# Kernel optimization log

Hardware: AMD Instinct MI355X
Metric: run time of the kernel (lower is better)

## Reference

```python
import jax, jax.numpy as jnp
import numpy as np


def setup_inputs() -> dict:
    key = jax.random.key(0)
    ks = jax.random.split(key, 5)
    T, C_IN, C_OUT, H = 1024, 4, 2, 32
    x = jax.random.normal(ks[0], (T, C_IN), dtype=jnp.float32)
    # timestamps (relative positions); arange normalized to [0,1)
    t = jnp.arange(T, dtype=jnp.float32) / T
    # KernelNet params: Linear(3,H) -> Sine -> Linear(H,1)
    w1 = jax.random.normal(ks[1], (H, 3), dtype=jnp.float32) * (1.0 / np.sqrt(3.0))
    b1 = jax.random.normal(ks[2], (H,), dtype=jnp.float32) * 0.1
    w2 = jax.random.normal(ks[3], (1, H), dtype=jnp.float32) * (1.0 / np.sqrt(H))
    b2 = jax.random.normal(ks[4], (1,), dtype=jnp.float32) * 0.1
    return {"x": x, "t": t, "w1": w1, "b1": b1, "w2": w2, "b2": b2,
            "out_channels": C_OUT}


def reference(x, t, w1, b1, w2, b2, out_channels):
    # x: [T, C_in], t: [T]
    T, C_in = x.shape
    # dt[i, j] = t[j] - t[i]  (rep_t - rep_t.t() in the original)
    dt = t[None, :] - t[:, None]                                  # [T, T]
    # Kernel MLP input is [dt, in_channel_idx, out_channel_idx]; the first
    # Linear layer is affine, so split contributions: dt*w1[:,0] varies over
    # (i, j) while the channel-index part varies only over (o, c).
    h_dt = dt[:, :, None] * w1[:, 0]                              # [T, T, H]
    c_idx = jnp.arange(C_in, dtype=x.dtype)                       # [C_in]
    o_idx = jnp.arange(out_channels, dtype=x.dtype)               # [C_out]
    off = (o_idx[:, None, None] * w1[:, 2]
           + c_idx[None, :, None] * w1[:, 1]
           + b1)                                                  # [O, C, H]
    h = jnp.sin(h_dt[None, None] + off[:, :, None, None, :])      # [O, C, T, T, H]
    kernel = jnp.einsum('ocijh,h->ocij', h, w2[0]) + b2[0]        # [O, C, T, T]
    # causal mask: keep entries with j <= i (lower triangular), tiled per (o, c)
    mask = jnp.tril(jnp.ones((T, T), dtype=x.dtype))
    kernel = kernel * mask
    # y[i, o] = sum_{c, j<=i} kernel[o, c, i, j] * x[j, c]
    return jnp.einsum('ocij,jc->io', kernel, x)                   # [T, O]
```

## Files before the change

kernel.cpp:

```cpp
#include <hip/hip_runtime.h>
#include <math.h>

__global__ void ck_build_kernel_table(const float* __restrict__ t,
                                      const float* __restrict__ w1,
                                      const float* __restrict__ b1,
                                      const float* __restrict__ w2,
                                      const float* __restrict__ b2,
                                      float* __restrict__ Kt,
                                      int T, int Cin, int Cout, int H) {
    int idx = blockIdx.x * blockDim.x + threadIdx.x;
    int total = T * Cout * Cin;
    if (idx >= total) return;
    int oc  = Cout * Cin;
    int d   = idx / oc;
    int rem = idx - d * oc;
    int o   = rem / Cin;
    int c   = rem - o * Cin;

    float dt = t[0] - t[d];
    float fo = (float)o;
    float fc = (float)c;

    float acc = 0.0f;
    for (int h = 0; h < H; ++h) {
        float a = dt * w1[h * 3 + 0] + fc * w1[h * 3 + 1] + fo * w1[h * 3 + 2] + b1[h];
        acc += w2[h] * sinf(a);
    }
    Kt[idx] = acc + b2[0];
}

__global__ __launch_bounds__(256) void ck_causal_conv(
        const float* __restrict__ x,
        const float* __restrict__ Kt,
        float* __restrict__ out,
        int T) {
    const int i = blockIdx.x;
    float acc0 = 0.0f, acc1 = 0.0f;

    for (int j = threadIdx.x; j <= i; j += 256) {
        const int d = i - j;
        const float4 xv = *reinterpret_cast<const float4*>(x + j * 4);
        const float4 k0 = *reinterpret_cast<const float4*>(Kt + d * 8);
        const float4 k1 = *reinterpret_cast<const float4*>(Kt + d * 8 + 4);
        acc0 += k0.x * xv.x + k0.y * xv.y + k0.z * xv.z + k0.w * xv.w;
        acc1 += k1.x * xv.x + k1.y * xv.y + k1.z * xv.z + k1.w * xv.w;
    }

    #pragma unroll
    for (int off = 32; off > 0; off >>= 1) {
        acc0 += __shfl_down(acc0, off, 64);
        acc1 += __shfl_down(acc1, off, 64);
    }

    __shared__ float s0[4], s1[4];
    const int lane = threadIdx.x & 63;
    const int wid  = threadIdx.x >> 6;
    if (lane == 0) { s0[wid] = acc0; s1[wid] = acc1; }
    __syncthreads();
    if (threadIdx.x == 0) {
        float a = s0[0] + s0[1] + s0[2] + s0[3];
        float b = s1[0] + s1[1] + s1[2] + s1[3];
        out[i * 2 + 0] = a;
        out[i * 2 + 1] = b;
    }
}

extern "C" void kernel_launch(void* const* d_in, const int* in_sizes, int n_in,
                              void* d_out, int out_size, void* d_ws, size_t ws_size,
                              hipStream_t stream) {
    const float* x  = (const float*)d_in[0];
    const float* t  = (const float*)d_in[1];
    const float* w1 = (const float*)d_in[2];
    const float* b1 = (const float*)d_in[3];
    const float* w2 = (const float*)d_in[4];
    const float* b2 = (const float*)d_in[5];
    float* out = (float*)d_out;

    const int T    = in_sizes[1];
    const int Cin  = in_sizes[0] / T;
    const int H    = in_sizes[3];
    const int Cout = out_size / T;

    float* Kt = (float*)d_ws;

    const int total   = T * Cout * Cin;
    const int blocks1 = (total + 255) / 256;
    ck_build_kernel_table<<<blocks1, 256, 0, stream>>>(t, w1, b1, w2, b2, Kt,
                                                       T, Cin, Cout, H);
    ck_causal_conv<<<T, 256, 0, stream>>>(x, Kt, out, T);
}
```

Baseline: 73.85 us.

## Share sincos across channel pairs via angle-addition in kernel table build

```diff
diff --git a/kernel.cpp b/kernel.cpp
--- a/kernel.cpp
+++ b/kernel.cpp
@@ -1,32 +1,61 @@
 #include <hip/hip_runtime.h>
 #include <math.h>
 
-__global__ void ck_build_kernel_table(const float* __restrict__ t,
-                                      const float* __restrict__ w1,
-                                      const float* __restrict__ b1,
-                                      const float* __restrict__ w2,
-                                      const float* __restrict__ b2,
-                                      float* __restrict__ Kt,
-                                      int T, int Cin, int Cout, int H) {
-    int idx = blockIdx.x * blockDim.x + threadIdx.x;
-    int total = T * Cout * Cin;
-    if (idx >= total) return;
-    int oc  = Cout * Cin;
-    int d   = idx / oc;
-    int rem = idx - d * oc;
-    int o   = rem / Cin;
-    int c   = rem - o * Cin;
+__global__ __launch_bounds__(256) void ck_build_kernel_table(
+        const float* __restrict__ t,
+        const float* __restrict__ w1,
+        const float* __restrict__ b1,
+        const float* __restrict__ w2,
+        const float* __restrict__ b2,
+        float* __restrict__ Kt,
+        int T, int H) {
+    __shared__ float cphi[32 * 8];
+    __shared__ float sphi[32 * 8];
+    __shared__ float w2s[32];
+    __shared__ float wfreq[32];
 
-    float dt = t[0] - t[d];
-    float fo = (float)o;
-    float fc = (float)c;
+    const int tid = threadIdx.x;
+    if (tid < H * 8) {
+        const int h  = tid >> 3;
+        const int oc = tid & 7;
+        const float fo = (float)(oc >> 2);
+        const float fc = (float)(oc & 3);
+        const float phi = fo * w1[h * 3 + 2] + fc * w1[h * 3 + 1] + b1[h];
+        cphi[tid] = cosf(phi);
+        sphi[tid] = sinf(phi);
+    }
+    if (tid < H) {
+        w2s[tid]   = w2[tid];
+        wfreq[tid] = w1[tid * 3 + 0];
+    }
+    __syncthreads();
 
-    float acc = 0.0f;
+    const int d = blockIdx.x * 256 + tid;
+    if (d >= T) return;
+
+    const float dt  = t[0] - t[d];
+    const float b2v = b2[0];
+
+    float acc[8];
+    #pragma unroll
+    for (int k = 0; k < 8; ++k) acc[k] = 0.0f;
+
     for (int h = 0; h < H; ++h) {
-        float a = dt * w1[h * 3 + 0] + fc * w1[h * 3 + 1] + fo * w1[h * 3 + 2] + b1[h];
-        acc += w2[h] * sinf(a);
+        float s, c;
+        sincosf(dt * wfreq[h], &s, &c);
+        const float w  = w2s[h];
+        const float ws = w * s;
+        const float wc = w * c;
+        #pragma unroll
+        for (int oc = 0; oc < 8; ++oc) {
+            acc[oc] += ws * cphi[h * 8 + oc] + wc * sphi[h * 8 + oc];
+        }
     }
-    Kt[idx] = acc + b2[0];
+
+    float4 v0 = make_float4(acc[0] + b2v, acc[1] + b2v, acc[2] + b2v, acc[3] + b2v);
+    float4 v1 = make_float4(acc[4] + b2v, acc[5] + b2v, acc[6] + b2v, acc[7] + b2v);
+    *reinterpret_cast<float4*>(Kt + d * 8)     = v0;
+    *reinterpret_cast<float4*>(Kt + d * 8 + 4) = v1;
 }
 
 __global__ __launch_bounds__(256) void ck_causal_conv(
@@ -58,10 +87,8 @@
     if (lane == 0) { s0[wid] = acc0; s1[wid] = acc1; }
     __syncthreads();
     if (threadIdx.x == 0) {
-        float a = s0[0] + s0[1] + s0[2] + s0[3];
-        float b = s1[0] + s1[1] + s1[2] + s1[3];
-        out[i * 2 + 0] = a;
-        out[i * 2 + 1] = b;
+        out[i * 2 + 0] = s0[0] + s0[1] + s0[2] + s0[3];
+        out[i * 2 + 1] = s1[0] + s1[1] + s1[2] + s1[3];
     }
 }
 
@@ -76,16 +103,12 @@
     const float* b2 = (const float*)d_in[5];
     float* out = (float*)d_out;
 
-    const int T    = in_sizes[1];
-    const int Cin  = in_sizes[0] / T;
-    const int H    = in_sizes[3];
-    const int Cout = out_size / T;
+    const int T = in_sizes[1];
+    const int H = in_sizes[3];
 
     float* Kt = (float*)d_ws;
 
-    const int total   = T * Cout * Cin;
-    const int blocks1 = (total + 255) / 256;
-    ck_build_kernel_table<<<blocks1, 256, 0, stream>>>(t, w1, b1, w2, b2, Kt,
-                                                       T, Cin, Cout, H);
+    const int blocks1 = (T + 255) / 256;
+    ck_build_kernel_table<<<blocks1, 256, 0, stream>>>(t, w1, b1, w2, b2, Kt, T, H);
     ck_causal_conv<<<T, 256, 0, stream>>>(x, Kt, out, T);
 }
```

After: 74.31 us. About the same (+0.6%).
